# Kernel tuning notes

Hardware: AMD Instinct MI355X
Metric: run time of the kernel (lower is better)

## Reference

```python
import jax, jax.numpy as jnp
import numpy as np

TOP_K = 8
ALPHA = 0.1
EPS = 1e-20


def setup_inputs() -> dict:
    key = jax.random.key(0)
    k1, k2 = jax.random.split(key)
    B, S, D, E = 4, 8192, 1024, 64
    hidden_states = jax.random.normal(k1, (B, S, D), dtype=jnp.float32)
    # kaiming_uniform_(a=sqrt(5)) on [E, D] -> bound = 1/sqrt(D)
    bound = 1.0 / np.sqrt(D)
    W = jax.random.uniform(k2, (E, D), dtype=jnp.float32, minval=-bound, maxval=bound)
    return {"hidden_states": hidden_states, "W": W}


def reference(hidden_states, W):
    B, S, D = hidden_states.shape
    E = W.shape[0]
    x = hidden_states.reshape(-1, D)                       # [T, D], T = B*S
    logits = jnp.einsum('td,ed->te', x, W)                 # [T, E]
    scores = jax.nn.softmax(logits, axis=-1)               # [T, E]
    top_k_weights, top_k_idx = jax.lax.top_k(scores, TOP_K)  # [T, K]
    # norm_topk_experts renormalization
    top_k_weights = top_k_weights / (top_k_weights.sum(axis=-1, keepdims=True) + EPS)
    # seq_aux loss: per-batch expert selection counts via scatter-add
    idx = top_k_idx.reshape(B, -1)                         # [B, S*K]
    ce = jnp.zeros((B, E), dtype=jnp.float32).at[jnp.arange(B)[:, None], idx].add(1.0)
    mean_scores = scores.reshape(B, S, E).mean(axis=1)     # [B, E]
    aux_loss = (ce * mean_scores).sum(axis=1).mean() * ALPHA
    return top_k_idx, top_k_weights, aux_loss
```

## Files before the change

### kernel.cpp

```cpp
#include <hip/hip_runtime.h>

#define TOKS   32768
#define NEXP   64
#define DDIM   1024
#define SEQ    8192
#define NBATCH 4
#define TPB    64
#define STR    68
#define CSTR   21

__global__ __launch_bounds__(256, 2) void moe_gate_main(
    const float* __restrict__ X, const float* __restrict__ W,
    float* __restrict__ out, float* __restrict__ gsum, float* __restrict__ gce,
    int* __restrict__ flag_cnt, int* __restrict__ flag_tok)
{
  __shared__ __align__(16) float xs[64 * STR];
  __shared__ __align__(16) float wsm[64 * STR];
  __shared__ float red[256];
  __shared__ float gmx[64];
  __shared__ float cval[64 * CSTR];
  __shared__ int   cidx[64 * CSTR];
  __shared__ int   hist[NEXP];

  const int tid = threadIdx.x;
  const int tok_base = blockIdx.x * TPB;
  const int bb = blockIdx.x >> 7;

  const int lc = tid & 15;
  const int lr = tid >> 4;
  const int l  = tid & 63;
  const int q  = tid >> 6;
  const int t0c = (l >> 3) * 8;
  const int e0c = (l & 7) * 8;
  const int dq = q * 16;
  const int pcol = (4 * lr + 4 * lc) & 63;

  float acc[8][8];
#pragma unroll
  for (int i = 0; i < 8; ++i)
#pragma unroll
    for (int j = 0; j < 8; ++j) acc[i][j] = 0.0f;

  float4 px[4], pw[4];
#pragma unroll
  for (int i = 0; i < 4; ++i) {
    px[i] = *(const float4*)(X + (size_t)(tok_base + 4 * lr + i) * DDIM + 4 * lc);
    pw[i] = *(const float4*)(W + (size_t)(4 * lr + i) * DDIM + 4 * lc);
  }

#pragma unroll 1
  for (int kt = 0; kt < DDIM / 64; ++kt) {
    __syncthreads();
#pragma unroll
    for (int j = 0; j < 4; ++j) {
      float4 vx = make_float4(((const float*)&px[0])[j], ((const float*)&px[1])[j],
                              ((const float*)&px[2])[j], ((const float*)&px[3])[j]);
      float4 vw = make_float4(((const float*)&pw[0])[j], ((const float*)&pw[1])[j],
                              ((const float*)&pw[2])[j], ((const float*)&pw[3])[j]);
      *(float4*)&xs[(4 * lc + j) * 64 + pcol] = vx;
      *(float4*)&wsm[(4 * lc + j) * 64 + pcol] = vw;
    }
    __syncthreads();
    if (kt + 1 < DDIM / 64) {
      const int dbase = (kt + 1) * 64;
#pragma unroll
      for (int i = 0; i < 4; ++i) {
        px[i] = *(const float4*)(X + (size_t)(tok_base + 4 * lr + i) * DDIM + dbase + 4 * lc);
        pw[i] = *(const float4*)(W + (size_t)(4 * lr + i) * DDIM + dbase + 4 * lc);
      }
    }
#pragma unroll
    for (int d = 0; d < 16; ++d) {
      const int row = dq + d;
      const int rot = dq + (d & 12);
      const float* xr = &xs[row * 64];
      const float* wr = &wsm[row * 64];
      float xv[8], wv[8];
      *(float4*)&xv[0] = *(const float4*)(xr + ((t0c + rot) & 63));
      *(float4*)&xv[4] = *(const float4*)(xr + ((t0c + 4 + rot) & 63));
      *(float4*)&wv[0] = *(const float4*)(wr + ((e0c + rot) & 63));
      *(float4*)&wv[4] = *(const float4*)(wr + ((e0c + 4 + rot) & 63));
#pragma unroll
      for (int i = 0; i < 8; ++i)
#pragma unroll
        for (int j = 0; j < 8; ++j)
          acc[i][j] = fmaf(xv[i], wv[j], acc[i][j]);
    }
  }

  __syncthreads();
  if (q == 2) {
#pragma unroll
    for (int i = 0; i < 8; ++i) {
      *(float4*)&xs[(t0c + i) * STR + e0c]     = *(float4*)&acc[i][0];
      *(float4*)&xs[(t0c + i) * STR + e0c + 4] = *(float4*)&acc[i][4];
    }
  }
  if (q == 3) {
#pragma unroll
    for (int i = 0; i < 8; ++i) {
      *(float4*)&wsm[(t0c + i) * STR + e0c]     = *(float4*)&acc[i][0];
      *(float4*)&wsm[(t0c + i) * STR + e0c + 4] = *(float4*)&acc[i][4];
    }
  }
  __syncthreads();
  if (q == 0) {
#pragma unroll
    for (int i = 0; i < 8; ++i) {
      float4 a = *(const float4*)&xs[(t0c + i) * STR + e0c];
      float4 b = *(const float4*)&xs[(t0c + i) * STR + e0c + 4];
      acc[i][0] += a.x; acc[i][1] += a.y; acc[i][2] += a.z; acc[i][3] += a.w;
      acc[i][4] += b.x; acc[i][5] += b.y; acc[i][6] += b.z; acc[i][7] += b.w;
    }
  }
  if (q == 1) {
#pragma unroll
    for (int i = 0; i < 8; ++i) {
      float4 a = *(const float4*)&wsm[(t0c + i) * STR + e0c];
      float4 b = *(const float4*)&wsm[(t0c + i) * STR + e0c + 4];
      acc[i][0] += a.x; acc[i][1] += a.y; acc[i][2] += a.z; acc[i][3] += a.w;
      acc[i][4] += b.x; acc[i][5] += b.y; acc[i][6] += b.z; acc[i][7] += b.w;
    }
  }
  __syncthreads();
  if (q == 1) {
#pragma unroll
    for (int i = 0; i < 8; ++i) {
      *(float4*)&xs[(t0c + i) * STR + e0c]     = *(float4*)&acc[i][0];
      *(float4*)&xs[(t0c + i) * STR + e0c + 4] = *(float4*)&acc[i][4];
    }
  }
  __syncthreads();
  if (q == 0) {
#pragma unroll
    for (int i = 0; i < 8; ++i) {
      float4 a = *(const float4*)&xs[(t0c + i) * STR + e0c];
      float4 b = *(const float4*)&xs[(t0c + i) * STR + e0c + 4];
      acc[i][0] += a.x; acc[i][1] += a.y; acc[i][2] += a.z; acc[i][3] += a.w;
      acc[i][4] += b.x; acc[i][5] += b.y; acc[i][6] += b.z; acc[i][7] += b.w;
      *(float4*)&wsm[(t0c + i) * STR + e0c]     = *(float4*)&acc[i][0];
      *(float4*)&wsm[(t0c + i) * STR + e0c + 4] = *(float4*)&acc[i][4];
    }
    hist[l] = 0;
  }
  __syncthreads();

  float* logits  = wsm;
  float* scoresT = xs;
  const int t = l;

  float m = -__builtin_huge_valf();
#pragma unroll
  for (int e = 0; e < 16; ++e) m = fmaxf(m, logits[t * STR + q * 16 + e]);
  red[q * 64 + t] = m;
  __syncthreads();
  float gm = fmaxf(fmaxf(red[t], red[64 + t]), fmaxf(red[128 + t], red[192 + t]));
  if (q == 0) gmx[t] = gm;
  float z = 0.0f;
#pragma unroll
  for (int e = 0; e < 16; ++e) {
    float ev = expf(logits[t * STR + q * 16 + e] - gm);
    scoresT[(q * 16 + e) * STR + t] = ev;
    z += ev;
  }
  __syncthreads();
  red[q * 64 + t] = z;
  __syncthreads();
  float Z = red[t] + red[64 + t] + red[128 + t] + red[192 + t];
  float invZ = 1.0f / Z;
#pragma unroll
  for (int e = 0; e < 16; ++e) scoresT[(q * 16 + e) * STR + t] *= invZ;
  __syncthreads();

  {
    const int e = l, g = q;
    float s = 0.0f;
#pragma unroll
    for (int tt = 0; tt < 16; ++tt) s += scoresT[e * STR + g * 16 + tt];
    red[g * 64 + e] = s;
  }
  __syncthreads();
  if (tid < 64) {
    float tot = red[tid] + red[64 + tid] + red[128 + tid] + red[192 + tid];
    atomicAdd(&gsum[bb * 64 + tid], tot);
  }

  if (tid < 128) {
    const int h = tid >> 6;
    const int eb = h * 32;
#pragma unroll 1
    for (int k = 0; k < 9; ++k) {
      float mv = -1.0f; int mi = eb;
#pragma unroll 4
      for (int e = 0; e < 32; ++e) {
        float v = scoresT[(eb + e) * STR + t];
        if (v > mv) { mv = v; mi = eb + e; }
      }
      cval[t * CSTR + h * 9 + k] = mv;
      cidx[t * CSTR + h * 9 + k] = mi;
      scoresT[mi * STR + t] = -1.0f;
    }
  }
  __syncthreads();

  if (tid < 64) {
    float wv[9]; int wi[8];
#pragma unroll 1
    for (int k = 0; k < 9; ++k) {
      float mv = -1.0f; int mj = 0;
#pragma unroll 3
      for (int j = 0; j < 18; ++j) {
        float v = cval[t * CSTR + j];
        if (v > mv) { mv = v; mj = j; }
      }
      wv[k] = mv;
      if (k < 8) {
        wi[k] = cidx[t * CSTR + mj];
        atomicAdd(&hist[wi[k]], 1);
      }
      cval[t * CSTR + mj] = -1.0f;
    }
    bool flag = false;
#pragma unroll
    for (int k = 0; k < 8; ++k)
      if (wv[k + 1] >= wv[k] * (1.0f - 2.0e-5f)) flag = true;
    if (flag) {
      int p = atomicAdd(flag_cnt, 1);
      flag_tok[p] = tok_base + t;
    }
    double ed[8]; double den = 0.0;
#pragma unroll
    for (int k = 0; k < 8; ++k) {
      ed[k] = exp((double)logits[t * STR + wi[k]] - (double)gmx[t]);
      den += ed[k];
    }
    const size_t tg = (size_t)(tok_base + t);
    *(float4*)(out + tg * 8) =
        make_float4((float)wi[0], (float)wi[1], (float)wi[2], (float)wi[3]);
    *(float4*)(out + tg * 8 + 4) =
        make_float4((float)wi[4], (float)wi[5], (float)wi[6], (float)wi[7]);
    *(float4*)(out + (size_t)TOKS * 8 + tg * 8) =
        make_float4((float)(ed[0] / den), (float)(ed[1] / den),
                    (float)(ed[2] / den), (float)(ed[3] / den));
    *(float4*)(out + (size_t)TOKS * 8 + tg * 8 + 4) =
        make_float4((float)(ed[4] / den), (float)(ed[5] / den),
                    (float)(ed[6] / den), (float)(ed[7] / den));
  }
  __syncthreads();
  if (tid < 64) atomicAdd(&gce[bb * 64 + tid], (float)hist[tid]);
}

__global__ __launch_bounds__(256) void moe_refine(
    const float* __restrict__ X, const float* __restrict__ W,
    float* __restrict__ out, float* __restrict__ gce,
    const int* __restrict__ flag_cnt, const int* __restrict__ flag_tok)
{
  __shared__ __align__(16) float xrow[DDIM];
  __shared__ double part[4][NEXP];
  const int tid = threadIdx.x;
  const int n = *flag_cnt;
  const int e = tid & 63;
  const int c = tid >> 6;
#pragma unroll 1
  for (int it = blockIdx.x; it < n; it += 256) {
    const int tok = flag_tok[it];
    __syncthreads();
    *(float4*)&xrow[tid * 4] = *(const float4*)&X[(size_t)tok * DDIM + tid * 4];
    __syncthreads();
    const float* wr = W + (size_t)e * DDIM + c * 256;
    const float* xr = xrow + c * 256;
    double s0 = 0.0, s1 = 0.0, s2 = 0.0, s3 = 0.0;
#pragma unroll 4
    for (int j = 0; j < 256; j += 4) {
      s0 += (double)xr[j]     * (double)wr[j];
      s1 += (double)xr[j + 1] * (double)wr[j + 1];
      s2 += (double)xr[j + 2] * (double)wr[j + 2];
      s3 += (double)xr[j + 3] * (double)wr[j + 3];
    }
    part[c][e] = (s0 + s1) + (s2 + s3);
    __syncthreads();
    if (tid < 64) {
      double cur = (part[0][e] + part[1][e]) + (part[2][e] + part[3][e]);
      int wi[8]; double wl[8];
#pragma unroll 1
      for (int k = 0; k < 8; ++k) {
        double mv = cur; int mi = e;
#pragma unroll
        for (int off = 1; off < 64; off <<= 1) {
          double ov = __shfl_xor(mv, off);
          int    oi = __shfl_xor(mi, off);
          if (ov > mv || (ov == mv && oi < mi)) { mv = ov; mi = oi; }
        }
        wi[k] = mi; wl[k] = mv;
        if (e == mi) cur = -1.0e300;
      }
      if (e == 0) {
        int olde[8];
#pragma unroll
        for (int k = 0; k < 8; ++k) olde[k] = (int)out[(size_t)tok * 8 + k];
        double ex[8]; double den = 0.0;
#pragma unroll
        for (int k = 0; k < 8; ++k) { ex[k] = exp(wl[k] - wl[0]); den += ex[k]; }
#pragma unroll
        for (int k = 0; k < 8; ++k) {
          out[(size_t)tok * 8 + k] = (float)wi[k];
          out[(size_t)TOKS * 8 + (size_t)tok * 8 + k] = (float)(ex[k] / den);
        }
        const int bbb = tok >> 13;
#pragma unroll 1
        for (int k = 0; k < 8; ++k) {
          bool in_new = false, in_old = false;
          for (int j = 0; j < 8; ++j) {
            if (wi[j] == olde[k]) in_new = true;
            if (olde[j] == wi[k]) in_old = true;
          }
          if (!in_new) atomicAdd(&gce[bbb * 64 + olde[k]], -1.0f);
          if (!in_old) atomicAdd(&gce[bbb * 64 + wi[k]], 1.0f);
        }
      }
    }
  }
}

__global__ void moe_gate_aux(const float* __restrict__ gsum,
                             const float* __restrict__ gce,
                             float* __restrict__ out)
{
  __shared__ float r[256];
  const int tid = threadIdx.x;
  r[tid] = gce[tid] * gsum[tid];
  __syncthreads();
  for (int s = 128; s > 0; s >>= 1) {
    if (tid < s) r[tid] += r[tid + s];
    __syncthreads();
  }
  if (tid == 0)
    out[(size_t)TOKS * 16] = 0.1f * r[0] / ((float)SEQ * (float)NBATCH);
}

extern "C" void kernel_launch(void* const* d_in, const int* in_sizes, int n_in,
                              void* d_out, int out_size, void* d_ws, size_t ws_size,
                              hipStream_t stream)
{
  const float* X = (const float*)d_in[0];
  const float* W = (const float*)d_in[1];
  float* out  = (float*)d_out;
  float* gsum = (float*)d_ws;
  float* gce  = gsum + NBATCH * NEXP;
  int* flag_cnt = (int*)((char*)d_ws + 2048);
  int* flag_tok = (int*)((char*)d_ws + 2176);

  hipMemsetAsync(d_ws, 0, 2176, stream);
  moe_gate_main<<<TOKS / TPB, 256, 0, stream>>>(X, W, out, gsum, gce, flag_cnt, flag_tok);
  moe_refine<<<256, 256, 0, stream>>>(X, W, out, gce, flag_cnt, flag_tok);
  moe_gate_aux<<<1, 256, 0, stream>>>(gsum, gce, out);
}
```

Measured before the change: 241.8 us.

## Compute gate logits with split-bf16 MFMA instead of FP32 FMA

Replaces the scalar FP32 outer-product GEMM for the router logits with bf16 MFMA 16x16x32 instructions. Each FP32 value is split into high and low bf16 parts, and three MFMAs (hh, lh, hl) approximate FP32 accuracy. The K-tile grows to 128 and the cross-warp K-split reduction goes away, since each wave now owns a 32x32 output tile. This trades extra conversion work in the staging path and a small loss of precision, which could change top-k choices on near-ties, for much higher matrix throughput.

```diff
diff --git a/kernel.cpp b/kernel.cpp
--- a/kernel.cpp
+++ b/kernel.cpp
@@ -1,4 +1,5 @@
 #include <hip/hip_runtime.h>
+#include <hip/hip_bf16.h>
 
 #define TOKS   32768
 #define NEXP   64
@@ -8,141 +9,131 @@
 #define TPB    64
 #define STR    68
 #define CSTR   21
+#define BK     128
+#define NCH    (DDIM / BK)
+#define ASTR   136
+
+typedef __attribute__((ext_vector_type(8))) short short8v;
+typedef __attribute__((ext_vector_type(4))) float f32x4;
+
+__device__ __forceinline__ void stage4(ushort* dh, ushort* dl, float4 v) {
+  __hip_bfloat162 h0 = __float22bfloat162_rn(make_float2(v.x, v.y));
+  __hip_bfloat162 h1 = __float22bfloat162_rn(make_float2(v.z, v.w));
+  float2 f0 = __bfloat1622float2(h0);
+  float2 f1 = __bfloat1622float2(h1);
+  __hip_bfloat162 l0 = __float22bfloat162_rn(make_float2(v.x - f0.x, v.y - f0.y));
+  __hip_bfloat162 l1 = __float22bfloat162_rn(make_float2(v.z - f1.x, v.w - f1.y));
+  *(__hip_bfloat162*)(dh)     = h0;
+  *(__hip_bfloat162*)(dh + 2) = h1;
+  *(__hip_bfloat162*)(dl)     = l0;
+  *(__hip_bfloat162*)(dl + 2) = l1;
+}
 
 __global__ __launch_bounds__(256, 2) void moe_gate_main(
     const float* __restrict__ X, const float* __restrict__ W,
     float* __restrict__ out, float* __restrict__ gsum, float* __restrict__ gce,
     int* __restrict__ flag_cnt, int* __restrict__ flag_tok)
 {
-  __shared__ __align__(16) float xs[64 * STR];
-  __shared__ __align__(16) float wsm[64 * STR];
-  __shared__ float red[256];
-  __shared__ float gmx[64];
-  __shared__ float cval[64 * CSTR];
-  __shared__ int   cidx[64 * CSTR];
-  __shared__ int   hist[NEXP];
+  __shared__ __align__(16) char smem[4 * 64 * ASTR * 2];
+
+  ushort* Ah = (ushort*)smem;
+  ushort* Al = Ah + 64 * ASTR;
+  ushort* Bh = Al + 64 * ASTR;
+  ushort* Bl = Bh + 64 * ASTR;
+
+  float* xs   = (float*)smem;
+  float* wsm  = (float*)(smem + 17408);
+  float* red  = (float*)(smem + 34816);
+  float* gmx  = (float*)(smem + 35840);
+  float* cval = (float*)(smem + 36096);
+  int*   cidx = (int*)  (smem + 41472);
+  int*   hist = (int*)  (smem + 46848);
 
   const int tid = threadIdx.x;
   const int tok_base = blockIdx.x * TPB;
   const int bb = blockIdx.x >> 7;
 
-  const int lc = tid & 15;
-  const int lr = tid >> 4;
-  const int l  = tid & 63;
-  const int q  = tid >> 6;
-  const int t0c = (l >> 3) * 8;
-  const int e0c = (l & 7) * 8;
-  const int dq = q * 16;
-  const int pcol = (4 * lr + 4 * lc) & 63;
-
-  float acc[8][8];
-#pragma unroll
-  for (int i = 0; i < 8; ++i)
-#pragma unroll
-    for (int j = 0; j < 8; ++j) acc[i][j] = 0.0f;
-
-  float4 px[4], pw[4];
-#pragma unroll
-  for (int i = 0; i < 4; ++i) {
-    px[i] = *(const float4*)(X + (size_t)(tok_base + 4 * lr + i) * DDIM + 4 * lc);
-    pw[i] = *(const float4*)(W + (size_t)(4 * lr + i) * DDIM + 4 * lc);
-  }
-
-#pragma unroll 1
-  for (int kt = 0; kt < DDIM / 64; ++kt) {
-    __syncthreads();
-#pragma unroll
-    for (int j = 0; j < 4; ++j) {
-      float4 vx = make_float4(((const float*)&px[0])[j], ((const float*)&px[1])[j],
-                              ((const float*)&px[2])[j], ((const float*)&px[3])[j]);
-      float4 vw = make_float4(((const float*)&pw[0])[j], ((const float*)&pw[1])[j],
-                              ((const float*)&pw[2])[j], ((const float*)&pw[3])[j]);
-      *(float4*)&xs[(4 * lc + j) * 64 + pcol] = vx;
-      *(float4*)&wsm[(4 * lc + j) * 64 + pcol] = vw;
-    }
-    __syncthreads();
-    if (kt + 1 < DDIM / 64) {
-      const int dbase = (kt + 1) * 64;
-#pragma unroll
-      for (int i = 0; i < 4; ++i) {
-        px[i] = *(const float4*)(X + (size_t)(tok_base + 4 * lr + i) * DDIM + dbase + 4 * lc);
-        pw[i] = *(const float4*)(W + (size_t)(4 * lr + i) * DDIM + dbase + 4 * lc);
-      }
-    }
-#pragma unroll
-    for (int d = 0; d < 16; ++d) {
-      const int row = dq + d;
-      const int rot = dq + (d & 12);
-      const float* xr = &xs[row * 64];
-      const float* wr = &wsm[row * 64];
-      float xv[8], wv[8];
-      *(float4*)&xv[0] = *(const float4*)(xr + ((t0c + rot) & 63));
-      *(float4*)&xv[4] = *(const float4*)(xr + ((t0c + 4 + rot) & 63));
-      *(float4*)&wv[0] = *(const float4*)(wr + ((e0c + rot) & 63));
-      *(float4*)&wv[4] = *(const float4*)(wr + ((e0c + 4 + rot) & 63));
-#pragma unroll
-      for (int i = 0; i < 8; ++i)
-#pragma unroll
-        for (int j = 0; j < 8; ++j)
-          acc[i][j] = fmaf(xv[i], wv[j], acc[i][j]);
-    }
-  }
-
-  __syncthreads();
-  if (q == 2) {
+  const int l = tid & 63;
+  const int q = tid >> 6;
+
+  const int c4 = tid & 31;
+  const int r0 = tid >> 5;
+
+  const int wm = q >> 1, wn = q & 1;
+  const int fr = l & 15;
+  const int fk = (l >> 4) * 8;
+
+  f32x4 accA[2][2], accB[2][2];
+#pragma unroll
+  for (int i = 0; i < 2; ++i)
+#pragma unroll
+    for (int j = 0; j < 2; ++j) {
+      accA[i][j] = (f32x4)0.0f;
+      accB[i][j] = (f32x4)0.0f;
+    }
+
+  float4 px[8], pw[8];
+#pragma unroll
+  for (int i = 0; i < 8; ++i) {
+    px[i] = *(const float4*)(X + (size_t)(tok_base + r0 + 8 * i) * DDIM + 4 * c4);
+    pw[i] = *(const float4*)(W + (size_t)(r0 + 8 * i) * DDIM + 4 * c4);
+  }
+
+#pragma unroll 1
+  for (int kt = 0; kt < NCH; ++kt) {
+    __syncthreads();
 #pragma unroll
     for (int i = 0; i < 8; ++i) {
-      *(float4*)&xs[(t0c + i) * STR + e0c]     = *(float4*)&acc[i][0];
-      *(float4*)&xs[(t0c + i) * STR + e0c + 4] = *(float4*)&acc[i][4];
-    }
-  }
-  if (q == 3) {
-#pragma unroll
-    for (int i = 0; i < 8; ++i) {
-      *(float4*)&wsm[(t0c + i) * STR + e0c]     = *(float4*)&acc[i][0];
-      *(float4*)&wsm[(t0c + i) * STR + e0c + 4] = *(float4*)&acc[i][4];
-    }
-  }
-  __syncthreads();
-  if (q == 0) {
-#pragma unroll
-    for (int i = 0; i < 8; ++i) {
-      float4 a = *(const float4*)&xs[(t0c + i) * STR + e0c];
-      float4 b = *(const float4*)&xs[(t0c + i) * STR + e0c + 4];
-      acc[i][0] += a.x; acc[i][1] += a.y; acc[i][2] += a.z; acc[i][3] += a.w;
-      acc[i][4] += b.x; acc[i][5] += b.y; acc[i][6] += b.z; acc[i][7] += b.w;
-    }
-  }
-  if (q == 1) {
-#pragma unroll
-    for (int i = 0; i < 8; ++i) {
-      float4 a = *(const float4*)&wsm[(t0c + i) * STR + e0c];
-      float4 b = *(const float4*)&wsm[(t0c + i) * STR + e0c + 4];
-      acc[i][0] += a.x; acc[i][1] += a.y; acc[i][2] += a.z; acc[i][3] += a.w;
-      acc[i][4] += b.x; acc[i][5] += b.y; acc[i][6] += b.z; acc[i][7] += b.w;
-    }
-  }
-  __syncthreads();
-  if (q == 1) {
-#pragma unroll
-    for (int i = 0; i < 8; ++i) {
-      *(float4*)&xs[(t0c + i) * STR + e0c]     = *(float4*)&acc[i][0];
-      *(float4*)&xs[(t0c + i) * STR + e0c + 4] = *(float4*)&acc[i][4];
-    }
-  }
-  __syncthreads();
-  if (q == 0) {
-#pragma unroll
-    for (int i = 0; i < 8; ++i) {
-      float4 a = *(const float4*)&xs[(t0c + i) * STR + e0c];
-      float4 b = *(const float4*)&xs[(t0c + i) * STR + e0c + 4];
-      acc[i][0] += a.x; acc[i][1] += a.y; acc[i][2] += a.z; acc[i][3] += a.w;
-      acc[i][4] += b.x; acc[i][5] += b.y; acc[i][6] += b.z; acc[i][7] += b.w;
-      *(float4*)&wsm[(t0c + i) * STR + e0c]     = *(float4*)&acc[i][0];
-      *(float4*)&wsm[(t0c + i) * STR + e0c + 4] = *(float4*)&acc[i][4];
-    }
-    hist[l] = 0;
-  }
+      const int row = r0 + 8 * i;
+      stage4(&Ah[row * ASTR + 4 * c4], &Al[row * ASTR + 4 * c4], px[i]);
+      stage4(&Bh[row * ASTR + 4 * c4], &Bl[row * ASTR + 4 * c4], pw[i]);
+    }
+    __syncthreads();
+    if (kt + 1 < NCH) {
+      const int db = (kt + 1) * BK;
+#pragma unroll
+      for (int i = 0; i < 8; ++i) {
+        px[i] = *(const float4*)(X + (size_t)(tok_base + r0 + 8 * i) * DDIM + db + 4 * c4);
+        pw[i] = *(const float4*)(W + (size_t)(r0 + 8 * i) * DDIM + db + 4 * c4);
+      }
+    }
+#pragma unroll
+    for (int s = 0; s < BK / 32; ++s) {
+      const int ko = s * 32 + fk;
+      short8v a_h[2], a_l[2], b_h[2], b_l[2];
+#pragma unroll
+      for (int i = 0; i < 2; ++i) {
+        const ushort* pa = Ah + (size_t)(32 * wm + 16 * i + fr) * ASTR + ko;
+        a_h[i] = *(const short8v*)pa;
+        a_l[i] = *(const short8v*)(pa + 64 * ASTR);
+        const ushort* pb = Bh + (size_t)(32 * wn + 16 * i + fr) * ASTR + ko;
+        b_h[i] = *(const short8v*)pb;
+        b_l[i] = *(const short8v*)(pb + 64 * ASTR);
+      }
+#pragma unroll
+      for (int i = 0; i < 2; ++i)
+#pragma unroll
+        for (int j = 0; j < 2; ++j) {
+          accA[i][j] = __builtin_amdgcn_mfma_f32_16x16x32_bf16(a_h[i], b_h[j], accA[i][j], 0, 0, 0);
+          accB[i][j] = __builtin_amdgcn_mfma_f32_16x16x32_bf16(a_l[i], b_h[j], accB[i][j], 0, 0, 0);
+          accA[i][j] = __builtin_amdgcn_mfma_f32_16x16x32_bf16(a_h[i], b_l[j], accA[i][j], 0, 0, 0);
+        }
+    }
+  }
+
+  __syncthreads();
+#pragma unroll
+  for (int i = 0; i < 2; ++i)
+#pragma unroll
+    for (int j = 0; j < 2; ++j) {
+      f32x4 c = accA[i][j] + accB[i][j];
+      const int tok = 32 * wm + 16 * i + 4 * (l >> 4);
+      const int e   = 32 * wn + 16 * j + fr;
+#pragma unroll
+      for (int r = 0; r < 4; ++r)
+        wsm[(tok + r) * STR + e] = c[r];
+    }
+  if (tid < 64) hist[tid] = 0;
   __syncthreads();
 
   float* logits  = wsm;
```

Result: faster. 228.1 us (-5.7%).
